# Performance work log

Measured on AMD Instinct MI355X. Metric: run time of the kernel, lower is better.

Reference implementation:

```python
import jax, jax.numpy as jnp
import numpy as np

NUM_CLASSES = 16384
FEAT_DIM = 1024
ALPHA = 0.5


def setup_inputs() -> dict:
    key = jax.random.key(0)
    k1, k2, k3 = jax.random.split(key, 3)
    y_true = jax.random.randint(k1, (NUM_CLASSES,), 0, NUM_CLASSES, dtype=jnp.int32)
    y_pred = jax.random.normal(k2, (NUM_CLASSES, FEAT_DIM), dtype=jnp.float32)
    centers = jax.random.normal(k3, (NUM_CLASSES, FEAT_DIM), dtype=jnp.float32)
    return {"y_true": y_true, "y_pred": y_pred, "centers": centers}


def reference(y_true, y_pred, centers):
    # gather current centers per sample: [B, D]
    delta_centers = centers[y_true] - y_pred
    # per-class counts, gathered back per sample (tf.math.bincount semantics,
    # static length = NUM_CLASSES since all indices < NUM_CLASSES)
    counts = jnp.bincount(y_true, length=NUM_CLASSES)
    per_sample_counts = counts[y_true].astype(y_pred.dtype)  # [B]
    delta_centers = ALPHA * delta_centers / (per_sample_counts[:, None] + 1.0)
    # original code does an elementwise assign_sub (requires B == num_classes)
    new_centers = centers - delta_centers
    # MSE between features and the freshly-updated gathered centers
    diff = y_pred - new_centers[y_true]
    loss = jnp.mean(jnp.square(diff))
    return loss
```

## Files before the change

### kernel.cpp

```cpp
#include <hip/hip_runtime.h>

#define B 16384
#define D 1024
#define CL_ALPHA 0.5f
#define MAXM 16

__global__ void build_kernel(const int* __restrict__ y_true,
                             int* __restrict__ counts,
                             int* __restrict__ list) {
    int i = blockIdx.x * blockDim.x + threadIdx.x;
    if (i >= B) return;
    int j = y_true[i];
    int slot = atomicAdd(&counts[j], 1);
    if (slot < MAXM) list[j * MAXM + slot] = i;
}

__global__ void prep_kernel(const int* __restrict__ y_true,
                            const int* __restrict__ counts,
                            int* __restrict__ n_work,
                            int4* __restrict__ meta) {
    int j = blockIdx.x * blockDim.x + threadIdx.x;
    if (j >= B) return;
    int m = counts[j];
    if (m == 0) return;
    if (m > MAXM) m = MAXM;
    int kk = y_true[j];
    float inv = CL_ALPHA / ((float)counts[kk] + 1.0f);
    int w = atomicAdd(n_work, 1);
    meta[w] = make_int4(j | (m << 20), kk, __float_as_int(inv), 0);
}

__global__ __launch_bounds__(256) void class_kernel(const float* __restrict__ y_pred,
                                                    const float* __restrict__ centers,
                                                    const int* __restrict__ n_work,
                                                    const int4* __restrict__ meta,
                                                    const int* __restrict__ list,
                                                    float* __restrict__ partials) {
    const int nw = *n_work;
    if ((int)blockIdx.x >= nw) return;

    const int4 me = meta[blockIdx.x];
    const int j  = me.x & 0xFFFFF;
    const int mm = me.x >> 20;
    const int kk = me.y;
    const float inv = __int_as_float(me.z);

    const int t = threadIdx.x;

    int idx[MAXM];
    #pragma unroll
    for (int s = 0; s < MAXM; ++s)
        idx[s] = (s < mm) ? list[j * MAXM + s] : 0;

    float4 cj = ((const float4*)(centers + (size_t)j  * D))[t];
    float4 ck = ((const float4*)(centers + (size_t)kk * D))[t];
    float4 yj = ((const float4*)(y_pred  + (size_t)j  * D))[t];
    float4 corr;
    corr.x = inv * (ck.x - yj.x) - cj.x;
    corr.y = inv * (ck.y - yj.y) - cj.y;
    corr.z = inv * (ck.z - yj.z) - cj.z;
    corr.w = inv * (ck.w - yj.w) - cj.w;

    float acc = 0.0f;
    for (int s = 0; s < mm; ++s) {
        float4 a = ((const float4*)(y_pred + (size_t)idx[s] * D))[t];
        float dx = a.x + corr.x;
        float dy = a.y + corr.y;
        float dz = a.z + corr.z;
        float dw = a.w + corr.w;
        acc += dx * dx + dy * dy + dz * dz + dw * dw;
    }

    #pragma unroll
    for (int off = 32; off > 0; off >>= 1)
        acc += __shfl_down(acc, off, 64);

    __shared__ float smem[4];
    const int lane = t & 63;
    const int wave = t >> 6;
    if (lane == 0) smem[wave] = acc;
    __syncthreads();
    if (t == 0)
        partials[blockIdx.x] = smem[0] + smem[1] + smem[2] + smem[3];
}

__global__ __launch_bounds__(1024) void finalize_kernel(const float* __restrict__ partials,
                                                        float* __restrict__ out) {
    const int t = threadIdx.x;
    const float4* p4 = (const float4*)partials;
    float acc = 0.0f;
    #pragma unroll
    for (int w = 0; w < 4; ++w) {
        float4 v = p4[t + 1024 * w];
        acc += v.x + v.y + v.z + v.w;
    }
    #pragma unroll
    for (int off = 32; off > 0; off >>= 1)
        acc += __shfl_down(acc, off, 64);

    __shared__ float smem[16];
    const int lane = t & 63;
    const int wave = t >> 6;
    if (lane == 0) smem[wave] = acc;
    __syncthreads();
    if (t == 0) {
        float s = 0.0f;
        #pragma unroll
        for (int w = 0; w < 16; ++w) s += smem[w];
        out[0] = s * (1.0f / ((float)B * (float)D));
    }
}

extern "C" void kernel_launch(void* const* d_in, const int* in_sizes, int n_in,
                              void* d_out, int out_size, void* d_ws, size_t ws_size,
                              hipStream_t stream) {
    const int*   y_true  = (const int*)d_in[0];
    const float* y_pred  = (const float*)d_in[1];
    const float* centers = (const float*)d_in[2];
    float* out = (float*)d_out;

    int*   counts   = (int*)d_ws;
    float* partials = (float*)(counts + B);
    int*   n_work   = (int*)(partials + B);
    int4*  meta     = (int4*)(n_work + 4);
    int*   list     = (int*)(meta + B);

    hipMemsetAsync(d_ws, 0, (size_t)(2 * B + 4) * sizeof(int), stream);

    build_kernel<<<B / 256, 256, 0, stream>>>(y_true, counts, list);
    prep_kernel<<<B / 256, 256, 0, stream>>>(y_true, counts, n_work, meta);
    class_kernel<<<B, 256, 0, stream>>>(y_pred, centers, n_work, meta, list, partials);
    finalize_kernel<<<1, 1024, 0, stream>>>(partials, out);
}
```

Before: 160.7 us.

## Map one work item per wavefront and unroll member loads

The class kernel now gives each work item (class) to a single 64-lane wavefront instead of a whole 256-thread block, so each block handles four classes and the grid shrinks by four. Each lane covers four float4 slices of the row, and the member loop is unrolled by two so more independent global loads are in flight per wave. This removes the shared-memory reduction and the __syncthreads, and cuts the number of blocks that launch only to exit early. In exchange, each thread holds more registers for the correction vectors and loaded rows. A block may also end up with uneven work when its waves have different member counts.

```diff
diff --git a/kernel.cpp b/kernel.cpp
--- a/kernel.cpp
+++ b/kernel.cpp
@@ -36,52 +36,74 @@
                                                     const int4* __restrict__ meta,
                                                     const int* __restrict__ list,
                                                     float* __restrict__ partials) {
-    const int nw = *n_work;
-    if ((int)blockIdx.x >= nw) return;
+    const int wave = threadIdx.x >> 6;
+    const int lane = threadIdx.x & 63;
+    const int e = blockIdx.x * 4 + wave;
+    if (e >= *n_work) return;
 
-    const int4 me = meta[blockIdx.x];
+    const int4 me = meta[e];
     const int j  = me.x & 0xFFFFF;
     const int mm = me.x >> 20;
     const int kk = me.y;
     const float inv = __int_as_float(me.z);
-
-    const int t = threadIdx.x;
 
     int idx[MAXM];
     #pragma unroll
     for (int s = 0; s < MAXM; ++s)
         idx[s] = (s < mm) ? list[j * MAXM + s] : 0;
 
-    float4 cj = ((const float4*)(centers + (size_t)j  * D))[t];
-    float4 ck = ((const float4*)(centers + (size_t)kk * D))[t];
-    float4 yj = ((const float4*)(y_pred  + (size_t)j  * D))[t];
-    float4 corr;
-    corr.x = inv * (ck.x - yj.x) - cj.x;
-    corr.y = inv * (ck.y - yj.y) - cj.y;
-    corr.z = inv * (ck.z - yj.z) - cj.z;
-    corr.w = inv * (ck.w - yj.w) - cj.w;
+    const float4* Cj = (const float4*)(centers + (size_t)j  * D);
+    const float4* Ck = (const float4*)(centers + (size_t)kk * D);
+    const float4* Yj = (const float4*)(y_pred  + (size_t)j  * D);
+
+    float4 cj0 = Cj[lane],       cj1 = Cj[lane + 64],  cj2 = Cj[lane + 128], cj3 = Cj[lane + 192];
+    float4 ck0 = Ck[lane],       ck1 = Ck[lane + 64],  ck2 = Ck[lane + 128], ck3 = Ck[lane + 192];
+    float4 yj0 = Yj[lane],       yj1 = Yj[lane + 64],  yj2 = Yj[lane + 128], yj3 = Yj[lane + 192];
+
+    float4 corr[4];
+#define MKCORR(q, ckv, yjv, cjv) \
+    corr[q].x = inv * (ckv.x - yjv.x) - cjv.x; \
+    corr[q].y = inv * (ckv.y - yjv.y) - cjv.y; \
+    corr[q].z = inv * (ckv.z - yjv.z) - cjv.z; \
+    corr[q].w = inv * (ckv.w - yjv.w) - cjv.w;
+    MKCORR(0, ck0, yj0, cj0)
+    MKCORR(1, ck1, yj1, cj1)
+    MKCORR(2, ck2, yj2, cj2)
+    MKCORR(3, ck3, yj3, cj3)
+#undef MKCORR
 
     float acc = 0.0f;
-    for (int s = 0; s < mm; ++s) {
-        float4 a = ((const float4*)(y_pred + (size_t)idx[s] * D))[t];
-        float dx = a.x + corr.x;
-        float dy = a.y + corr.y;
-        float dz = a.z + corr.z;
-        float dw = a.w + corr.w;
-        acc += dx * dx + dy * dy + dz * dz + dw * dw;
+#define ACCUM(Ap) do { \
+    float4 a0 = (Ap)[lane], a1 = (Ap)[lane + 64], a2 = (Ap)[lane + 128], a3 = (Ap)[lane + 192]; \
+    float dx, dy, dz, dw; \
+    dx = a0.x + corr[0].x; dy = a0.y + corr[0].y; dz = a0.z + corr[0].z; dw = a0.w + corr[0].w; \
+    acc += dx*dx + dy*dy + dz*dz + dw*dw; \
+    dx = a1.x + corr[1].x; dy = a1.y + corr[1].y; dz = a1.z + corr[1].z; dw = a1.w + corr[1].w; \
+    acc += dx*dx + dy*dy + dz*dz + dw*dw; \
+    dx = a2.x + corr[2].x; dy = a2.y + corr[2].y; dz = a2.z + corr[2].z; dw = a2.w + corr[2].w; \
+    acc += dx*dx + dy*dy + dz*dz + dw*dw; \
+    dx = a3.x + corr[3].x; dy = a3.y + corr[3].y; dz = a3.z + corr[3].z; dw = a3.w + corr[3].w; \
+    acc += dx*dx + dy*dy + dz*dz + dw*dw; \
+} while (0)
+
+    int s = 0;
+    for (; s + 2 <= mm; s += 2) {
+        const float4* A0 = (const float4*)(y_pred + (size_t)idx[s]     * D);
+        const float4* A1 = (const float4*)(y_pred + (size_t)idx[s + 1] * D);
+        ACCUM(A0);
+        ACCUM(A1);
     }
+    if (s < mm) {
+        const float4* A0 = (const float4*)(y_pred + (size_t)idx[s] * D);
+        ACCUM(A0);
+    }
+#undef ACCUM
 
     #pragma unroll
     for (int off = 32; off > 0; off >>= 1)
         acc += __shfl_down(acc, off, 64);
-
-    __shared__ float smem[4];
-    const int lane = t & 63;
-    const int wave = t >> 6;
-    if (lane == 0) smem[wave] = acc;
-    __syncthreads();
-    if (t == 0)
-        partials[blockIdx.x] = smem[0] + smem[1] + smem[2] + smem[3];
+    if (lane == 0)
+        partials[e] = acc;
 }
 
 __global__ __launch_bounds__(1024) void finalize_kernel(const float* __restrict__ partials,
@@ -129,6 +151,6 @@
 
     build_kernel<<<B / 256, 256, 0, stream>>>(y_true, counts, list);
     prep_kernel<<<B / 256, 256, 0, stream>>>(y_true, counts, n_work, meta);
-    class_kernel<<<B, 256, 0, stream>>>(y_pred, centers, n_work, meta, list, partials);
+    class_kernel<<<B / 4, 256, 0, stream>>>(y_pred, centers, n_work, meta, list, partials);
     finalize_kernel<<<1, 1024, 0, stream>>>(partials, out);
 }
```

Result: no change. 161.0 us (+0.2%).
